# Optimization experiments

Hardware: AMD Instinct MI355X
Metric: run time of the kernel (lower is better)

Reference implementation:

```python
import jax, jax.numpy as jnp
import numpy as np

B, N, D = 4, 4096, 1024

def setup_inputs() -> dict:
    key = jax.random.key(0)
    kx, kql, kqr, kk, kv = jax.random.split(key, 5)
    std = 1.0 / D
    return {
        "x": jax.random.normal(kx, (B, N, D), dtype=jnp.float32),
        "w_query_left": jax.random.normal(kql, (D, D), dtype=jnp.float32) * std,
        "w_query_right": jax.random.normal(kqr, (D, D), dtype=jnp.float32) * std,
        "w_key": jax.random.normal(kk, (D, D), dtype=jnp.float32) * std,
        "w_value": jax.random.normal(kv, (D, D), dtype=jnp.float32) * std,
    }

def reference(x, w_query_left, w_query_right, w_key, w_value):
    # Four dxd projections
    query_left = jnp.einsum('bnd,de->bne', x, w_query_left)
    query_right = jnp.einsum('bnd,de->bne', x, w_query_right)
    key = jnp.einsum('bnd,de->bne', x, w_key)
    value = jnp.einsum('bnd,de->bne', x, w_value)
    # Elementwise gate
    query = query_left * query_right
    # Kernelized attention: key^T @ value, then query @ kv  (dropout p=0 in eval)
    kv_attn = jnp.einsum('bnd,bne->bde', key, value)   # [B, D, D]
    linear_attn = jnp.einsum('bnd,bde->bne', query, kv_attn)
    return linear_attn
```

## Files before the change

### kernel.cpp

```cpp
#include <hip/hip_runtime.h>
#include <stdint.h>

typedef short bf16x8 __attribute__((ext_vector_type(8)));
typedef float f32x4 __attribute__((ext_vector_type(4)));

__device__ __forceinline__ uint16_t f2b(float f) {
    uint32_t u = __builtin_bit_cast(uint32_t, f);
    return (uint16_t)((u + 0x7fffu + ((u >> 16) & 1u)) >> 16);
}

__device__ __forceinline__ void gll16(const void* g, void* l) {
    __builtin_amdgcn_global_load_lds(
        (const __attribute__((address_space(1))) uint32_t*)(uintptr_t)g,
        (__attribute__((address_space(3))) uint32_t*)(uint32_t)(uintptr_t)l,
        16, 0, 0);
}

__global__ __launch_bounds__(256) void cvt_f32_bf16(const float4* __restrict__ in,
                                                    uint2* __restrict__ out, int nvec) {
    int i = blockIdx.x * 256 + threadIdx.x;
    if (i >= nvec) return;
    float4 v = in[i];
    uint2 o;
    o.x = (uint32_t)f2b(v.x) | ((uint32_t)f2b(v.y) << 16);
    o.y = (uint32_t)f2b(v.z) | ((uint32_t)f2b(v.w) << 16);
    out[i] = o;
}

struct Ptr4 { const float* p[4]; };

__global__ __launch_bounds__(256) void tr_w(Ptr4 wp, uint16_t* __restrict__ out) {
    const int m = blockIdx.z;
    const float* in = wp.p[m];
    uint16_t* o = out + (size_t)m * 1048576;
    __shared__ uint16_t tile[64][68];
    int t = threadIdx.x;
    int r0 = blockIdx.y * 64, c0 = blockIdx.x * 64;
    for (int p = 0; p < 4; p++) {
        int row = p * 16 + (t >> 4);
        int c4 = (t & 15) * 4;
        float4 v = *(const float4*)&in[(size_t)(r0 + row) * 1024 + c0 + c4];
        tile[row][c4 + 0] = f2b(v.x);
        tile[row][c4 + 1] = f2b(v.y);
        tile[row][c4 + 2] = f2b(v.z);
        tile[row][c4 + 3] = f2b(v.w);
    }
    __syncthreads();
    for (int p = 0; p < 4; p++) {
        int a = p * 16 + (t >> 4);
        int b4 = (t & 15) * 4;
        uint32_t x0 = tile[b4 + 0][a], x1 = tile[b4 + 1][a];
        uint32_t x2 = tile[b4 + 2][a], x3 = tile[b4 + 3][a];
        uint2 pk;
        pk.x = x0 | (x1 << 16);
        pk.y = x2 | (x3 << 16);
        *(uint2*)&o[(size_t)(c0 + a) * 1024 + r0 + b4] = pk;
    }
}

union SmemP {
    struct { uint16_t lA[4096]; uint16_t lB1[4096]; uint16_t lB2[4096]; } s;
    uint16_t tr[8][32][68];
};

__global__ __launch_bounds__(512, 4) void proj512(const uint16_t* __restrict__ A,
                                                  const uint16_t* __restrict__ Wt,
                                                  uint16_t* __restrict__ Q,
                                                  uint16_t* __restrict__ KT,
                                                  uint16_t* __restrict__ VT) {
    __shared__ SmemP u;
    const int t = threadIdx.x;
    const int wave = t >> 6;
    const int lane = t & 63;
    const int m0 = blockIdx.y * 128;
    const int bx = blockIdx.x;
    const int gate = bx < 8;
    const int e0 = (gate ? bx : bx - 8) * 128;
    const uint16_t* B1 = Wt + (size_t)(gate ? 0 : 2) * 1048576 + (size_t)e0 * 1024;
    const uint16_t* B2 = Wt + (size_t)(gate ? 1 : 3) * 1048576 + (size_t)e0 * 1024;
    const int wm = (wave >> 2) * 64;
    const int we = (wave & 3) * 32;

    const uint16_t* gA = A + (size_t)(m0 + (t >> 2)) * 1024 + (t & 3) * 8;
    const uint16_t* gB1 = B1 + (size_t)(t >> 2) * 1024 + (t & 3) * 8;
    const uint16_t* gB2 = B2 + (size_t)(t >> 2) * 1024 + (t & 3) * 8;
    uint16_t* dA = u.s.lA + wave * 512;
    uint16_t* dB1 = u.s.lB1 + wave * 512;
    uint16_t* dB2 = u.s.lB2 + wave * 512;

    f32x4 acc1[4][2] = {};
    f32x4 acc2[4][2] = {};

    const int arow = wm + (lane & 15);
    const int brow = we + (lane & 15);
    const int koff = (lane >> 4) * 8;

    for (int k0 = 0; k0 < 1024; k0 += 32) {
        __syncthreads();
        gll16(gA + k0, dA);
        gll16(gB1 + k0, dB1);
        gll16(gB2 + k0, dB2);
        __syncthreads();

        bf16x8 af[4], b1f[2], b2f[2];
#pragma unroll
        for (int i = 0; i < 4; i++)
            af[i] = *(const bf16x8*)&u.s.lA[(arow + i * 16) * 32 + koff];
#pragma unroll
        for (int j = 0; j < 2; j++)
            b1f[j] = *(const bf16x8*)&u.s.lB1[(brow + j * 16) * 32 + koff];
#pragma unroll
        for (int j = 0; j < 2; j++)
            b2f[j] = *(const bf16x8*)&u.s.lB2[(brow + j * 16) * 32 + koff];
#pragma unroll
        for (int i = 0; i < 4; i++)
#pragma unroll
            for (int j = 0; j < 2; j++) {
                acc1[i][j] = __builtin_amdgcn_mfma_f32_16x16x32_bf16(af[i], b1f[j],
                                                                     acc1[i][j], 0, 0, 0);
                acc2[i][j] = __builtin_amdgcn_mfma_f32_16x16x32_bf16(af[i], b2f[j],
                                                                     acc2[i][j], 0, 0, 0);
            }
    }

    const int rl = (lane >> 4) * 4;
    const int cl = lane & 15;

    if (gate) {
#pragma unroll
        for (int i = 0; i < 4; i++)
#pragma unroll
            for (int j = 0; j < 2; j++)
#pragma unroll
                for (int r = 0; r < 4; r++) {
                    float g = acc1[i][j][r] * acc2[i][j][r];
                    Q[(size_t)(m0 + wm + i * 16 + rl + r) * 1024 + e0 + we + j * 16 + cl] = f2b(g);
                }
    } else {
        __syncthreads();
        const int batch = m0 >> 12;
        const int tok0 = (m0 & 4095) + wm;
        const int fbase = e0 + we;
        uint16_t* outs[2] = {KT, VT};
        for (int s = 0; s < 2; s++) {
            f32x4(*acc)[2] = (s == 0) ? acc1 : acc2;
#pragma unroll
            for (int i = 0; i < 4; i++)
#pragma unroll
                for (int j = 0; j < 2; j++) {
                    int col = j * 16 + cl;
                    int row0 = i * 16 + rl;
                    uint2 pk;
                    pk.x = (uint32_t)f2b(acc[i][j][0]) | ((uint32_t)f2b(acc[i][j][1]) << 16);
                    pk.y = (uint32_t)f2b(acc[i][j][2]) | ((uint32_t)f2b(acc[i][j][3]) << 16);
                    *(uint2*)&u.tr[wave][col][row0] = pk;
                }
            __builtin_amdgcn_s_waitcnt(0);
            uint16_t* O = outs[s] + (size_t)batch * 4194304;
#pragma unroll
            for (int dd = 0; dd < 8; dd++) {
                int f = dd * 4 + (lane >> 4);
                int t4 = cl * 4;
                uint2 v = *(const uint2*)&u.tr[wave][f][t4];
                *(uint2*)&O[(size_t)(fbase + f) * 4096 + tok0 + t4] = v;
            }
            __builtin_amdgcn_s_waitcnt(0);
        }
    }
}

__global__ __launch_bounds__(256) void gemm_kv_splitk(const uint16_t* __restrict__ VT,
                                                      const uint16_t* __restrict__ KT,
                                                      float* __restrict__ P) {
    const int z = blockIdx.z;
    const int batch = z >> 1, ks = z & 1;
    const uint16_t* Ab = VT + (size_t)batch * 4194304 + ks * 2048;
    const uint16_t* Bb = KT + (size_t)batch * 4194304 + ks * 2048;

    __shared__ uint16_t lA[4096];
    __shared__ uint16_t lB[4096];

    const int t = threadIdx.x;
    const int wave = t >> 6;
    const int lane = t & 63;
    const int m0 = blockIdx.y * 128;
    const int n0 = blockIdx.x * 128;
    const int wm = (wave >> 1) * 64;
    const int wn = (wave & 1) * 64;

    const uint16_t* gA0 = Ab + (size_t)(m0 + (t >> 2)) * 4096 + (t & 3) * 8;
    const uint16_t* gB0 = Bb + (size_t)(n0 + (t >> 2)) * 4096 + (t & 3) * 8;
    uint16_t* lA0 = lA + wave * 512;
    uint16_t* lA1 = lA + 2048 + wave * 512;
    uint16_t* lB0 = lB + wave * 512;
    uint16_t* lB1 = lB + 2048 + wave * 512;

    f32x4 acc[4][4] = {};

    const int arow = wm + (lane & 15);
    const int brow = wn + (lane & 15);
    const int koff = (lane >> 4) * 8;

    for (int k0 = 0; k0 < 2048; k0 += 32) {
        __syncthreads();
        gll16(gA0 + k0, lA0);
        gll16(gA0 + (size_t)64 * 4096 + k0, lA1);
        gll16(gB0 + k0, lB0);
        gll16(gB0 + (size_t)64 * 4096 + k0, lB1);
        __syncthreads();

        bf16x8 af[4], bfr[4];
#pragma unroll
        for (int i = 0; i < 4; i++)
            af[i] = *(const bf16x8*)&lA[(arow + i * 16) * 32 + koff];
#pragma unroll
        for (int i = 0; i < 4; i++)
            bfr[i] = *(const bf16x8*)&lB[(brow + i * 16) * 32 + koff];
#pragma unroll
        for (int i = 0; i < 4; i++)
#pragma unroll
            for (int j = 0; j < 4; j++)
                acc[i][j] = __builtin_amdgcn_mfma_f32_16x16x32_bf16(af[i], bfr[j],
                                                                    acc[i][j], 0, 0, 0);
    }

    float* Pb = P + (size_t)z * 1048576;
    const int crow = m0 + wm + (lane >> 4) * 4;
    const int ccol = n0 + wn + (lane & 15);
#pragma unroll
    for (int i = 0; i < 4; i++)
#pragma unroll
        for (int j = 0; j < 4; j++)
#pragma unroll
            for (int r = 0; r < 4; r++)
                Pb[(size_t)(crow + i * 16 + r) * 1024 + ccol + j * 16] = acc[i][j][r];
}

__global__ __launch_bounds__(256) void reduce_kv(const float4* __restrict__ P,
                                                 uint2* __restrict__ kvT) {
    int i = blockIdx.x * 256 + threadIdx.x;
    int b = i >> 18;
    int r = i & 262143;
    const float4* base = P + (size_t)b * 524288 + r;
    float4 s0 = base[0];
    float4 s1 = base[262144];
    float x = s0.x + s1.x;
    float y = s0.y + s1.y;
    float zz = s0.z + s1.z;
    float w = s0.w + s1.w;
    uint2 o;
    o.x = (uint32_t)f2b(x) | ((uint32_t)f2b(y) << 16);
    o.y = (uint32_t)f2b(zz) | ((uint32_t)f2b(w) << 16);
    kvT[i] = o;
}

__global__ __launch_bounds__(256) void gemm_out(const uint16_t* __restrict__ A,
                                                const uint16_t* __restrict__ Bt,
                                                float* __restrict__ C) {
    const uint16_t* Ab = A + (size_t)blockIdx.z * 4194304;
    const uint16_t* Bb = Bt + (size_t)blockIdx.z * 1048576;

    __shared__ uint16_t lA[4096];
    __shared__ uint16_t lB[4096];

    const int t = threadIdx.x;
    const int wave = t >> 6;
    const int lane = t & 63;
    const int m0 = blockIdx.y * 128;
    const int n0 = blockIdx.x * 128;
    const int wm = (wave >> 1) * 64;
    const int wn = (wave & 1) * 64;

    const uint16_t* gA0 = Ab + (size_t)(m0 + (t >> 2)) * 1024 + (t & 3) * 8;
    const uint16_t* gB0 = Bb + (size_t)(n0 + (t >> 2)) * 1024 + (t & 3) * 8;
    uint16_t* lA0 = lA + wave * 512;
    uint16_t* lA1 = lA + 2048 + wave * 512;
    uint16_t* lB0 = lB + wave * 512;
    uint16_t* lB1 = lB + 2048 + wave * 512;

    f32x4 acc[4][4] = {};

    const int arow = wm + (lane & 15);
    const int brow = wn + (lane & 15);
    const int koff = (lane >> 4) * 8;

    for (int k0 = 0; k0 < 1024; k0 += 32) {
        __syncthreads();
        gll16(gA0 + k0, lA0);
        gll16(gA0 + (size_t)64 * 1024 + k0, lA1);
        gll16(gB0 + k0, lB0);
        gll16(gB0 + (size_t)64 * 1024 + k0, lB1);
        __syncthreads();

        bf16x8 af[4], bfr[4];
#pragma unroll
        for (int i = 0; i < 4; i++)
            af[i] = *(const bf16x8*)&lA[(arow + i * 16) * 32 + koff];
#pragma unroll
        for (int i = 0; i < 4; i++)
            bfr[i] = *(const bf16x8*)&lB[(brow + i * 16) * 32 + koff];
#pragma unroll
        for (int i = 0; i < 4; i++)
#pragma unroll
            for (int j = 0; j < 4; j++)
                acc[i][j] = __builtin_amdgcn_mfma_f32_16x16x32_bf16(af[i], bfr[j],
                                                                    acc[i][j], 0, 0, 0);
    }

    float* Cb = C + (size_t)blockIdx.z * 4194304;
    const int crow = m0 + wm + (lane >> 4) * 4;
    const int ccol = n0 + wn + (lane & 15);
#pragma unroll
    for (int i = 0; i < 4; i++)
#pragma unroll
        for (int j = 0; j < 4; j++)
#pragma unroll
            for (int r = 0; r < 4; r++)
                Cb[(size_t)(crow + i * 16 + r) * 1024 + ccol + j * 16] = acc[i][j][r];
}

extern "C" void kernel_launch(void* const* d_in, const int* in_sizes, int n_in,
                              void* d_out, int out_size, void* d_ws, size_t ws_size,
                              hipStream_t stream) {
    const float* x = (const float*)d_in[0];

    uint16_t* ws = (uint16_t*)d_ws;
    uint16_t* xb  = ws;
    float*    kvP = (float*)d_ws;
    uint16_t* Wt  = ws + 33554432;
    uint16_t* kvT = Wt;
    uint16_t* Q   = ws + 37748736;
    uint16_t* KT  = ws + 54525952;
    uint16_t* VT  = ws + 71303168;

    cvt_f32_bf16<<<16384, 256, 0, stream>>>((const float4*)x, (uint2*)xb, 4194304);

    Ptr4 wp;
    wp.p[0] = (const float*)d_in[1];
    wp.p[1] = (const float*)d_in[2];
    wp.p[2] = (const float*)d_in[3];
    wp.p[3] = (const float*)d_in[4];
    tr_w<<<dim3(16, 16, 4), 256, 0, stream>>>(wp, Wt);

    proj512<<<dim3(16, 128), 512, 0, stream>>>(xb, Wt, Q, KT, VT);

    gemm_kv_splitk<<<dim3(8, 8, 8), 256, 0, stream>>>(VT, KT, kvP);

    reduce_kv<<<4096, 256, 0, stream>>>((const float4*)kvP, (uint2*)kvT);

    gemm_out<<<dim3(8, 32, 4), 256, 0, stream>>>(Q, kvT, (float*)d_out);
}
```

Before: 392.2 us.

## Compute KᵀV as Wkᵀ(XᵀX)Wv instead of projecting K and V

Drops the key and value projections. The kernel now builds a per-batch Gram matrix XᵀX from a transposed bf16 copy of x, produced by a new fused convert-and-transpose kernel. The Gram matrix is then multiplied by the key and value weights through a generic bf16 NT GEMM, giving the DxD kv matrix directly. The projection kernel now computes only the gated query. This reassociation cuts the FLOPs and memory traffic of the two full-size projections. In exchange it adds an extra transposed copy of x, two small GEMMs, and an extra bf16 rounding of the Gram and intermediate products, which may change numerical accuracy.

```diff
diff --git a/kernel.cpp b/kernel.cpp
--- a/kernel.cpp
+++ b/kernel.cpp
@@ -16,15 +16,43 @@
         16, 0, 0);
 }
 
-__global__ __launch_bounds__(256) void cvt_f32_bf16(const float4* __restrict__ in,
-                                                    uint2* __restrict__ out, int nvec) {
-    int i = blockIdx.x * 256 + threadIdx.x;
-    if (i >= nvec) return;
-    float4 v = in[i];
-    uint2 o;
-    o.x = (uint32_t)f2b(v.x) | ((uint32_t)f2b(v.y) << 16);
-    o.y = (uint32_t)f2b(v.z) | ((uint32_t)f2b(v.w) << 16);
-    out[i] = o;
+__global__ __launch_bounds__(256) void cvt_tr(const float* __restrict__ x,
+                                              uint16_t* __restrict__ xb,
+                                              uint16_t* __restrict__ xT) {
+    const int b = blockIdx.z;
+    const int n0 = blockIdx.y * 64;
+    const int d0 = blockIdx.x * 64;
+    __shared__ uint16_t tile[64][66];
+    const int t = threadIdx.x;
+    const float* xbase = x + (size_t)b * 4194304;
+#pragma unroll
+    for (int p = 0; p < 4; p++) {
+        int row = p * 16 + (t >> 4);
+        int c4 = (t & 15) * 4;
+        float4 v = *(const float4*)&xbase[(size_t)(n0 + row) * 1024 + d0 + c4];
+        uint16_t b0 = f2b(v.x), b1 = f2b(v.y), b2 = f2b(v.z), b3 = f2b(v.w);
+        tile[row][c4 + 0] = b0;
+        tile[row][c4 + 1] = b1;
+        tile[row][c4 + 2] = b2;
+        tile[row][c4 + 3] = b3;
+        uint2 pk;
+        pk.x = (uint32_t)b0 | ((uint32_t)b1 << 16);
+        pk.y = (uint32_t)b2 | ((uint32_t)b3 << 16);
+        *(uint2*)&xb[(size_t)(b * 4096 + n0 + row) * 1024 + d0 + c4] = pk;
+    }
+    __syncthreads();
+    uint16_t* oT = xT + (size_t)b * 4194304;
+#pragma unroll
+    for (int p = 0; p < 4; p++) {
+        int a = p * 16 + (t >> 4);
+        int b4 = (t & 15) * 4;
+        uint32_t x0 = tile[b4 + 0][a], x1 = tile[b4 + 1][a];
+        uint32_t x2 = tile[b4 + 2][a], x3 = tile[b4 + 3][a];
+        uint2 pk;
+        pk.x = x0 | (x1 << 16);
+        pk.y = x2 | (x3 << 16);
+        *(uint2*)&oT[(size_t)(d0 + a) * 4096 + n0 + b4] = pk;
+    }
 }
 
 struct Ptr4 { const float* p[4]; };
@@ -58,35 +86,28 @@
     }
 }
 
-union SmemP {
-    struct { uint16_t lA[4096]; uint16_t lB1[4096]; uint16_t lB2[4096]; } s;
-    uint16_t tr[8][32][68];
-};
-
-__global__ __launch_bounds__(512, 4) void proj512(const uint16_t* __restrict__ A,
-                                                  const uint16_t* __restrict__ Wt,
-                                                  uint16_t* __restrict__ Q,
-                                                  uint16_t* __restrict__ KT,
-                                                  uint16_t* __restrict__ VT) {
-    __shared__ SmemP u;
+struct SmemG { uint16_t lA[4096]; uint16_t lB1[4096]; uint16_t lB2[4096]; };
+
+__global__ __launch_bounds__(512, 4) void proj_gate(const uint16_t* __restrict__ A,
+                                                    const uint16_t* __restrict__ Wt,
+                                                    uint16_t* __restrict__ Q) {
+    __shared__ SmemG u;
     const int t = threadIdx.x;
     const int wave = t >> 6;
     const int lane = t & 63;
     const int m0 = blockIdx.y * 128;
-    const int bx = blockIdx.x;
-    const int gate = bx < 8;
-    const int e0 = (gate ? bx : bx - 8) * 128;
-    const uint16_t* B1 = Wt + (size_t)(gate ? 0 : 2) * 1048576 + (size_t)e0 * 1024;
-    const uint16_t* B2 = Wt + (size_t)(gate ? 1 : 3) * 1048576 + (size_t)e0 * 1024;
+    const int e0 = blockIdx.x * 128;
+    const uint16_t* B1 = Wt + (size_t)e0 * 1024;
+    const uint16_t* B2 = Wt + 1048576 + (size_t)e0 * 1024;
     const int wm = (wave >> 2) * 64;
     const int we = (wave & 3) * 32;
 
     const uint16_t* gA = A + (size_t)(m0 + (t >> 2)) * 1024 + (t & 3) * 8;
     const uint16_t* gB1 = B1 + (size_t)(t >> 2) * 1024 + (t & 3) * 8;
     const uint16_t* gB2 = B2 + (size_t)(t >> 2) * 1024 + (t & 3) * 8;
-    uint16_t* dA = u.s.lA + wave * 512;
-    uint16_t* dB1 = u.s.lB1 + wave * 512;
-    uint16_t* dB2 = u.s.lB2 + wave * 512;
+    uint16_t* dA = u.lA + wave * 512;
+    uint16_t* dB1 = u.lB1 + wave * 512;
+    uint16_t* dB2 = u.lB2 + wave * 512;
 
     f32x4 acc1[4][2] = {};
     f32x4 acc2[4][2] = {};
@@ -105,13 +126,13 @@
         bf16x8 af[4], b1f[2], b2f[2];
 #pragma unroll
         for (int i = 0; i < 4; i++)
-            af[i] = *(const bf16x8*)&u.s.lA[(arow + i * 16) * 32 + koff];
+            af[i] = *(const bf16x8*)&u.lA[(arow + i * 16) * 32 + koff];
 #pragma unroll
         for (int j = 0; j < 2; j++)
-            b1f[j] = *(const bf16x8*)&u.s.lB1[(brow + j * 16) * 32 + koff];
+            b1f[j] = *(const bf16x8*)&u.lB1[(brow + j * 16) * 32 + koff];
 #pragma unroll
         for (int j = 0; j < 2; j++)
-            b2f[j] = *(const bf16x8*)&u.s.lB2[(brow + j * 16) * 32 + koff];
+            b2f[j] = *(const bf16x8*)&u.lB2[(brow + j * 16) * 32 + koff];
 #pragma unroll
         for (int i = 0; i < 4; i++)
 #pragma unroll
@@ -125,48 +146,15 @@
 
     const int rl = (lane >> 4) * 4;
     const int cl = lane & 15;
-
-    if (gate) {
-#pragma unroll
-        for (int i = 0; i < 4; i++)
-#pragma unroll
-            for (int j = 0; j < 2; j++)
-#pragma unroll
-                for (int r = 0; r < 4; r++) {
-                    float g = acc1[i][j][r] * acc2[i][j][r];
-                    Q[(size_t)(m0 + wm + i * 16 + rl + r) * 1024 + e0 + we + j * 16 + cl] = f2b(g);
-                }
-    } else {
-        __syncthreads();
-        const int batch = m0 >> 12;
-        const int tok0 = (m0 & 4095) + wm;
-        const int fbase = e0 + we;
-        uint16_t* outs[2] = {KT, VT};
-        for (int s = 0; s < 2; s++) {
-            f32x4(*acc)[2] = (s == 0) ? acc1 : acc2;
-#pragma unroll
-            for (int i = 0; i < 4; i++)
-#pragma unroll
-                for (int j = 0; j < 2; j++) {
-                    int col = j * 16 + cl;
-                    int row0 = i * 16 + rl;
-                    uint2 pk;
-                    pk.x = (uint32_t)f2b(acc[i][j][0]) | ((uint32_t)f2b(acc[i][j][1]) << 16);
-                    pk.y = (uint32_t)f2b(acc[i][j][2]) | ((uint32_t)f2b(acc[i][j][3]) << 16);
-                    *(uint2*)&u.tr[wave][col][row0] = pk;
-                }
-            __builtin_amdgcn_s_waitcnt(0);
-            uint16_t* O = outs[s] + (size_t)batch * 4194304;
-#pragma unroll
-            for (int dd = 0; dd < 8; dd++) {
-                int f = dd * 4 + (lane >> 4);
-                int t4 = cl * 4;
-                uint2 v = *(const uint2*)&u.tr[wave][f][t4];
-                *(uint2*)&O[(size_t)(fbase + f) * 4096 + tok0 + t4] = v;
+#pragma unroll
+    for (int i = 0; i < 4; i++)
+#pragma unroll
+        for (int j = 0; j < 2; j++)
+#pragma unroll
+            for (int r = 0; r < 4; r++) {
+                float g = acc1[i][j][r] * acc2[i][j][r];
+                Q[(size_t)(m0 + wm + i * 16 + rl + r) * 1024 + e0 + we + j * 16 + cl] = f2b(g);
             }
-            __builtin_amdgcn_s_waitcnt(0);
-        }
-    }
 }
 
 __global__ __launch_bounds__(256) void gemm_kv_splitk(const uint16_t* __restrict__ VT,
@@ -237,7 +225,7 @@
 }
 
 __global__ __launch_bounds__(256) void reduce_kv(const float4* __restrict__ P,
-                                                 uint2* __restrict__ kvT) {
+                                                 uint2* __restrict__ G) {
     int i = blockIdx.x * 256 + threadIdx.x;
     int b = i >> 18;
     int r = i & 262143;
@@ -251,14 +239,17 @@
     uint2 o;
     o.x = (uint32_t)f2b(x) | ((uint32_t)f2b(y) << 16);
     o.y = (uint32_t)f2b(zz) | ((uint32_t)f2b(w) << 16);
-    kvT[i] = o;
-}
-
-__global__ __launch_bounds__(256) void gemm_out(const uint16_t* __restrict__ A,
-                                                const uint16_t* __restrict__ Bt,
-                                                float* __restrict__ C) {
-    const uint16_t* Ab = A + (size_t)blockIdx.z * 4194304;
-    const uint16_t* Bb = Bt + (size_t)blockIdx.z * 1048576;
+    G[i] = o;
+}
+
+__global__ __launch_bounds__(256) void gemm_nt_bf16(const uint16_t* __restrict__ A,
+                                                    int lda, int az,
+                                                    const uint16_t* __restrict__ Bt,
+                                                    int ldb,
+                                                    uint16_t* __restrict__ C,
+                                                    int ldc, int cz) {
+    const uint16_t* Ab = A + (size_t)blockIdx.z * az;
+    uint16_t* Cb = C + (size_t)blockIdx.z * cz;
 
     __shared__ uint16_t lA[4096];
     __shared__ uint16_t lB[4096];
@@ -271,6 +262,70 @@
     const int wm = (wave >> 1) * 64;
     const int wn = (wave & 1) * 64;
 
+    const uint16_t* gA0 = Ab + (size_t)(m0 + (t >> 2)) * lda + (t & 3) * 8;
+    const uint16_t* gB0 = Bt + (size_t)(n0 + (t >> 2)) * ldb + (t & 3) * 8;
+    uint16_t* lA0 = lA + wave * 512;
+    uint16_t* lA1 = lA + 2048 + wave * 512;
+    uint16_t* lB0 = lB + wave * 512;
+    uint16_t* lB1 = lB + 2048 + wave * 512;
+
+    f32x4 acc[4][4] = {};
+
+    const int arow = wm + (lane & 15);
+    const int brow = wn + (lane & 15);
+    const int koff = (lane >> 4) * 8;
+
+    for (int k0 = 0; k0 < 1024; k0 += 32) {
+        __syncthreads();
+        gll16(gA0 + k0, lA0);
+        gll16(gA0 + (size_t)64 * lda + k0, lA1);
+        gll16(gB0 + k0, lB0);
+        gll16(gB0 + (size_t)64 * ldb + k0, lB1);
+        __syncthreads();
+
+        bf16x8 af[4], bfr[4];
+#pragma unroll
+        for (int i = 0; i < 4; i++)
+            af[i] = *(const bf16x8*)&lA[(arow + i * 16) * 32 + koff];
+#pragma unroll
+        for (int i = 0; i < 4; i++)
+            bfr[i] = *(const bf16x8*)&lB[(brow + i * 16) * 32 + koff];
+#pragma unroll
+        for (int i = 0; i < 4; i++)
+#pragma unroll
+            for (int j = 0; j < 4; j++)
+                acc[i][j] = __builtin_amdgcn_mfma_f32_16x16x32_bf16(af[i], bfr[j],
+                                                                    acc[i][j], 0, 0, 0);
+    }
+
+    const int crow = m0 + wm + (lane >> 4) * 4;
+    const int ccol = n0 + wn + (lane & 15);
+#pragma unroll
+    for (int i = 0; i < 4; i++)
+#pragma unroll
+        for (int j = 0; j < 4; j++)
+#pragma unroll
+            for (int r = 0; r < 4; r++)
+                Cb[(size_t)(crow + i * 16 + r) * ldc + ccol + j * 16] = f2b(acc[i][j][r]);
+}
+
+__global__ __launch_bounds__(256) void gemm_out(const uint16_t* __restrict__ A,
+                                                const uint16_t* __restrict__ Bt,
+                                                float* __restrict__ C) {
+    const uint16_t* Ab = A + (size_t)blockIdx.z * 4194304;
+    const uint16_t* Bb = Bt + (size_t)blockIdx.z * 1048576;
+
+    __shared__ uint16_t lA[4096];
+    __shared__ uint16_t lB[4096];
+
+    const int t = threadIdx.x;
+    const int wave = t >> 6;
+    const int lane = t & 63;
+    const int m0 = blockIdx.y * 128;
+    const int n0 = blockIdx.x * 128;
+    const int wm = (wave >> 1) * 64;
+    const int wn = (wave & 1) * 64;
+
     const uint16_t* gA0 = Ab + (size_t)(m0 + (t >> 2)) * 1024 + (t & 3) * 8;
     const uint16_t* gB0 = Bb + (size_t)(n0 + (t >> 2)) * 1024 + (t & 3) * 8;
     uint16_t* lA0 = lA + wave * 512;
@@ -324,16 +379,17 @@
                               hipStream_t stream) {
     const float* x = (const float*)d_in[0];
 
-    uint16_t* ws = (uint16_t*)d_ws;
+    uint16_t* ws  = (uint16_t*)d_ws;
     uint16_t* xb  = ws;
-    float*    kvP = (float*)d_ws;
+    uint16_t* xT  = ws + 16777216;
     uint16_t* Wt  = ws + 33554432;
-    uint16_t* kvT = Wt;
     uint16_t* Q   = ws + 37748736;
-    uint16_t* KT  = ws + 54525952;
-    uint16_t* VT  = ws + 71303168;
-
-    cvt_f32_bf16<<<16384, 256, 0, stream>>>((const float4*)x, (uint2*)xb, 4194304);
+    float*    P   = (float*)(ws + 54525952);
+    uint16_t* G   = ws + 71303168;
+    uint16_t* H   = ws + 75497472;
+    uint16_t* kvT = ws + 79691776;
+
+    cvt_tr<<<dim3(16, 64, 4), 256, 0, stream>>>(x, xb, xT);
 
     Ptr4 wp;
     wp.p[0] = (const float*)d_in[1];
@@ -342,11 +398,18 @@
     wp.p[3] = (const float*)d_in[4];
     tr_w<<<dim3(16, 16, 4), 256, 0, stream>>>(wp, Wt);
 
-    proj512<<<dim3(16, 128), 512, 0, stream>>>(xb, Wt, Q, KT, VT);
-
-    gemm_kv_splitk<<<dim3(8, 8, 8), 256, 0, stream>>>(VT, KT, kvP);
-
-    reduce_kv<<<4096, 256, 0, stream>>>((const float4*)kvP, (uint2*)kvT);
+    proj_gate<<<dim3(8, 128), 512, 0, stream>>>(xb, Wt, Q);
+
+    gemm_kv_splitk<<<dim3(8, 8, 8), 256, 0, stream>>>(xT, xT, P);
+
+    reduce_kv<<<4096, 256, 0, stream>>>((const float4*)P, (uint2*)G);
+
+    gemm_nt_bf16<<<dim3(32, 8, 1), 256, 0, stream>>>(Wt + 3 * 1048576, 1024, 0,
+                                                     G, 1024, H, 4096, 0);
+
+    gemm_nt_bf16<<<dim3(8, 8, 4), 256, 0, stream>>>(H, 4096, 1024,
+                                                    Wt + 2 * 1048576, 1024,
+                                                    kvT, 1024, 1048576);
 
     gemm_out<<<dim3(8, 32, 4), 256, 0, stream>>>(Q, kvT, (float*)d_out);
 }
```

Measured after the change: 380.3 us. 3.0% less time.
